# Performance work log

Hardware: AMD Instinct MI355X
Metric: run time of the kernel (lower is better)

## Reference

```python
import jax, jax.numpy as jnp
import numpy as np

N_NODES = 50000
N_EDGES = 800000
D_IN = 128
D_OUT = 128


def setup_inputs() -> dict:
    key = jax.random.key(0)
    k1, k2, k3, k4, k5 = jax.random.split(key, 5)
    gain = float(np.sqrt(2.0))  # calculate_gain('relu')
    # xavier_uniform bound: gain * sqrt(6/(fan_in+fan_out))
    bound = gain * float(np.sqrt(6.0 / (D_IN + D_OUT)))
    feat = jax.random.normal(k1, (N_NODES, D_IN), dtype=jnp.float32)
    weight = jax.random.uniform(k2, (D_IN, D_OUT), minval=-bound, maxval=bound, dtype=jnp.float32)
    loop_weight = jax.random.uniform(k3, (D_IN, D_OUT), minval=-bound, maxval=bound, dtype=jnp.float32)
    h_bias = jnp.zeros((D_OUT,), dtype=jnp.float32)
    src = jax.random.randint(k4, (N_EDGES,), 0, N_NODES, dtype=jnp.int32)
    dst = jax.random.randint(k5, (N_EDGES,), 0, N_NODES, dtype=jnp.int32)
    return {"feat": feat, "weight": weight, "h_bias": h_bias,
            "loop_weight": loop_weight, "src": src, "dst": dst}


def reference(feat, weight, h_bias, loop_weight, src, dst):
    # message: m_e = feat[src_e] @ W ; aggregate: h_v = sum_{e: dst_e=v} m_e
    # (equivalently transform-then-gather, which avoids the [E, D] matmul)
    transformed = feat @ weight                    # [N, D_out]
    msgs = transformed[src]                        # [E, D_out] gather
    h = jax.ops.segment_sum(msgs, dst, num_segments=feat.shape[0])  # [N, D_out]
    h = h + h_bias                                 # bias
    h = h + feat @ loop_weight                     # self-loop
    # activation=None, dropout=0 -> identity
    return h
```

## Files before the change

### kernel.cpp

```cpp
#include <hip/hip_runtime.h>

#define D 128
#define CAP 64

typedef __attribute__((ext_vector_type(8))) short bf16x8;
typedef __attribute__((ext_vector_type(4))) float f32x4;

__device__ inline unsigned short f2bf_rne(float x) {
    unsigned u = __float_as_uint(x);
    return (unsigned short)((u + 0x7FFFu + ((u >> 16) & 1u)) >> 16);
}

__global__ __launch_bounds__(256) void prep_kernel(
    const float* __restrict__ W, const float* __restrict__ LW,
    unsigned short* __restrict__ Bt, int* __restrict__ cursor, int N)
{
    int tid = blockIdx.x * 256 + threadIdx.x;
    if (tid < 2 * D * D) {
        int n = tid >> 7;
        int k = tid & 127;
        float v = (n < D) ? W[(size_t)k * D + n] : LW[(size_t)k * D + (n - D)];
        Bt[(size_t)n * D + k] = f2bf_rne(v);
    }
    int j = tid - 2 * D * D;
    if (j >= 0 && j < N) cursor[j] = 0;
}

__global__ __launch_bounds__(256) void mfma_transform(
    const float* __restrict__ feat, const unsigned short* __restrict__ Bt,
    const float* __restrict__ bias, unsigned short* __restrict__ T,
    float* __restrict__ out, int N)
{
    const int wave = threadIdx.x >> 6;
    const int lane = threadIdx.x & 63;
    const int row0 = blockIdx.x * 16;
    const int m    = lane & 15;
    const int kg   = lane >> 4;

    int arow_idx = row0 + m;
    if (arow_idx >= N) arow_idx = N - 1;
    const float* arow = feat + (size_t)arow_idx * D;

    bf16x8 a[4];
#pragma unroll
    for (int ks = 0; ks < 4; ++ks) {
        const float4 f0 = *(const float4*)(arow + ks * 32 + kg * 8);
        const float4 f1 = *(const float4*)(arow + ks * 32 + kg * 8 + 4);
        bf16x8 v;
        v[0] = (short)f2bf_rne(f0.x); v[1] = (short)f2bf_rne(f0.y);
        v[2] = (short)f2bf_rne(f0.z); v[3] = (short)f2bf_rne(f0.w);
        v[4] = (short)f2bf_rne(f1.x); v[5] = (short)f2bf_rne(f1.y);
        v[6] = (short)f2bf_rne(f1.z); v[7] = (short)f2bf_rne(f1.w);
        a[ks] = v;
    }

    const int colbase = wave * 64;
    f32x4 acc[4];
#pragma unroll
    for (int t = 0; t < 4; ++t) acc[t] = (f32x4){0.f, 0.f, 0.f, 0.f};

#pragma unroll
    for (int t = 0; t < 4; ++t) {
        const unsigned short* brow = Bt + (size_t)(colbase + t * 16 + m) * D;
#pragma unroll
        for (int ks = 0; ks < 4; ++ks) {
            bf16x8 b = *(const bf16x8*)(brow + ks * 32 + kg * 8);
            acc[t] = __builtin_amdgcn_mfma_f32_16x16x32_bf16(a[ks], b, acc[t], 0, 0, 0);
        }
    }

#pragma unroll
    for (int t = 0; t < 4; ++t) {
        const int col = colbase + t * 16 + m;
#pragma unroll
        for (int r = 0; r < 4; ++r) {
            const int row = row0 + kg * 4 + r;
            if (row < N) {
                const float v = acc[t][r];
                if (col < D) {
                    T[(size_t)row * D + col] = f2bf_rne(v);
                } else {
                    const int c = col - D;
                    out[(size_t)row * D + c] = v + bias[c];
                }
            }
        }
    }
}

__global__ __launch_bounds__(256) void fill_kernel(
    const int* __restrict__ src, const int* __restrict__ dst,
    int* __restrict__ cursor, unsigned short* __restrict__ ebuf, int E)
{
    int e = blockIdx.x * 256 + threadIdx.x;
    if (e >= E) return;
    const int d = dst[e];
    int pos = atomicAdd(&cursor[d], 1);
    if (pos < CAP) ebuf[(size_t)d * CAP + pos] = (unsigned short)src[e];
}

__global__ __launch_bounds__(256) void gather_kernel(
    const unsigned short* __restrict__ ebuf, const int* __restrict__ cursor,
    const unsigned short* __restrict__ T, float* __restrict__ out, int N)
{
    const int node = (blockIdx.x * 256 + threadIdx.x) >> 6;
    const int lane = threadIdx.x & 63;
    if (node >= N) return;

    int deg = cursor[node];
    if (deg > CAP) deg = CAP;

    const unsigned* region = (const unsigned*)(ebuf + (size_t)node * CAP);
    const unsigned short* Tbase = T + 2 * lane;

    float ax = 0.f, ay = 0.f;

    for (int j = 0; j < deg; j += 8) {
        unsigned w[4];
#pragma unroll
        for (int k = 0; k < 4; ++k) w[k] = region[(j >> 1) + k];

        unsigned u[8];
#pragma unroll
        for (int k = 0; k < 8; ++k) {
            const unsigned s = (k & 1) ? (w[k >> 1] >> 16) : (w[k >> 1] & 0xFFFFu);
            u[k] = *(const unsigned*)(Tbase + (size_t)s * D);
        }
#pragma unroll
        for (int k = 0; k < 8; ++k) {
            const bool live = (j + k) < deg;
            const float vx = __uint_as_float(u[k] << 16);
            const float vy = __uint_as_float(u[k] & 0xFFFF0000u);
            ax += live ? vx : 0.f;
            ay += live ? vy : 0.f;
        }
    }

    float2* o = (float2*)(out + (size_t)node * D + 2 * lane);
    float2 cur = *o;
    cur.x += ax;
    cur.y += ay;
    *o = cur;
}

extern "C" void kernel_launch(void* const* d_in, const int* in_sizes, int n_in,
                              void* d_out, int out_size, void* d_ws, size_t ws_size,
                              hipStream_t stream) {
    const float* feat = (const float*)d_in[0];
    const float* W    = (const float*)d_in[1];
    const float* bias = (const float*)d_in[2];
    const float* LW   = (const float*)d_in[3];
    const int*   src  = (const int*)d_in[4];
    const int*   dst  = (const int*)d_in[5];
    float* out = (float*)d_out;

    const int N = in_sizes[0] / D;
    const int E = in_sizes[4];

    unsigned short* T    = (unsigned short*)d_ws;
    unsigned short* Bt   = T + (size_t)N * D;
    unsigned short* ebuf = Bt + 2 * D * D;
    int* cursor = (int*)(ebuf + (size_t)N * CAP);

    {
        const int work = 2 * D * D + N;
        prep_kernel<<<dim3((work + 255) / 256), 256, 0, stream>>>(W, LW, Bt, cursor, N);
    }

    fill_kernel<<<dim3((E + 255) / 256), 256, 0, stream>>>(src, dst, cursor, ebuf, E);

    mfma_transform<<<dim3((N + 15) / 16), 256, 0, stream>>>(feat, Bt, bias, T, out, N);

    gather_kernel<<<dim3((N + 3) / 4), 256, 0, stream>>>(ebuf, cursor, T, out, N);
}
```

Measured before the change: 199.3 us.

## Merge edge fill into transform kernel and defer self-loop add to gather

The edge-bucketing fill and the MFMA transform now run as one launch: the first block range does the matmul, and the remaining blocks bucket edges. Each edge chunk is scanned by 8 blocks, and each block handles only destinations of one residue class mod 8. This spreads the cursor atomics apart, at the cost of reading dst eight times. The self-loop product is kept as bf16 next to the message transform in a 256-wide buffer, and the gather kernel adds bias and self-loop before writing out once. That removes the fp32 read-modify-write of the output but lowers the precision of the self-loop term.

```diff
diff --git a/kernel.cpp b/kernel.cpp
--- a/kernel.cpp
+++ b/kernel.cpp
@@ -2,6 +2,7 @@
 
 #define D 128
 #define CAP 64
+#define FCHUNK 2048
 
 typedef __attribute__((ext_vector_type(8))) short bf16x8;
 typedef __attribute__((ext_vector_type(4))) float f32x4;
@@ -26,82 +27,83 @@
     if (j >= 0 && j < N) cursor[j] = 0;
 }
 
-__global__ __launch_bounds__(256) void mfma_transform(
+__global__ __launch_bounds__(256) void merged_kernel(
     const float* __restrict__ feat, const unsigned short* __restrict__ Bt,
-    const float* __restrict__ bias, unsigned short* __restrict__ T,
-    float* __restrict__ out, int N)
+    unsigned short* __restrict__ T2,
+    const int* __restrict__ src, const int* __restrict__ dst,
+    int* __restrict__ cursor, unsigned short* __restrict__ ebuf,
+    int N, int E, int gb_mfma)
 {
-    const int wave = threadIdx.x >> 6;
-    const int lane = threadIdx.x & 63;
-    const int row0 = blockIdx.x * 16;
-    const int m    = lane & 15;
-    const int kg   = lane >> 4;
+    if ((int)blockIdx.x < gb_mfma) {
+        const int wave = threadIdx.x >> 6;
+        const int lane = threadIdx.x & 63;
+        const int row0 = blockIdx.x * 16;
+        const int m    = lane & 15;
+        const int kg   = lane >> 4;
 
-    int arow_idx = row0 + m;
-    if (arow_idx >= N) arow_idx = N - 1;
-    const float* arow = feat + (size_t)arow_idx * D;
+        int arow_idx = row0 + m;
+        if (arow_idx >= N) arow_idx = N - 1;
+        const float* arow = feat + (size_t)arow_idx * D;
 
-    bf16x8 a[4];
+        bf16x8 a[4];
 #pragma unroll
-    for (int ks = 0; ks < 4; ++ks) {
-        const float4 f0 = *(const float4*)(arow + ks * 32 + kg * 8);
-        const float4 f1 = *(const float4*)(arow + ks * 32 + kg * 8 + 4);
-        bf16x8 v;
-        v[0] = (short)f2bf_rne(f0.x); v[1] = (short)f2bf_rne(f0.y);
-        v[2] = (short)f2bf_rne(f0.z); v[3] = (short)f2bf_rne(f0.w);
-        v[4] = (short)f2bf_rne(f1.x); v[5] = (short)f2bf_rne(f1.y);
-        v[6] = (short)f2bf_rne(f1.z); v[7] = (short)f2bf_rne(f1.w);
-        a[ks] = v;
-    }
+        for (int ks = 0; ks < 4; ++ks) {
+            const float4 f0 = *(const float4*)(arow + ks * 32 + kg * 8);
+            const float4 f1 = *(const float4*)(arow + ks * 32 + kg * 8 + 4);
+            bf16x8 v;
+            v[0] = (short)f2bf_rne(f0.x); v[1] = (short)f2bf_rne(f0.y);
+            v[2] = (short)f2bf_rne(f0.z); v[3] = (short)f2bf_rne(f0.w);
+            v[4] = (short)f2bf_rne(f1.x); v[5] = (short)f2bf_rne(f1.y);
+            v[6] = (short)f2bf_rne(f1.z); v[7] = (short)f2bf_rne(f1.w);
+            a[ks] = v;
+        }
 
-    const int colbase = wave * 64;
-    f32x4 acc[4];
+        const int colbase = wave * 64;
+        f32x4 acc[4];
 #pragma unroll
-    for (int t = 0; t < 4; ++t) acc[t] = (f32x4){0.f, 0.f, 0.f, 0.f};
+        for (int t = 0; t < 4; ++t) acc[t] = (f32x4){0.f, 0.f, 0.f, 0.f};
 
 #pragma unroll
-    for (int t = 0; t < 4; ++t) {
-        const unsigned short* brow = Bt + (size_t)(colbase + t * 16 + m) * D;
+        for (int t = 0; t < 4; ++t) {
+            const unsigned short* brow = Bt + (size_t)(colbase + t * 16 + m) * D;
 #pragma unroll
-        for (int ks = 0; ks < 4; ++ks) {
-            bf16x8 b = *(const bf16x8*)(brow + ks * 32 + kg * 8);
-            acc[t] = __builtin_amdgcn_mfma_f32_16x16x32_bf16(a[ks], b, acc[t], 0, 0, 0);
+            for (int ks = 0; ks < 4; ++ks) {
+                bf16x8 b = *(const bf16x8*)(brow + ks * 32 + kg * 8);
+                acc[t] = __builtin_amdgcn_mfma_f32_16x16x32_bf16(a[ks], b, acc[t], 0, 0, 0);
+            }
         }
-    }
 
 #pragma unroll
-    for (int t = 0; t < 4; ++t) {
-        const int col = colbase + t * 16 + m;
+        for (int t = 0; t < 4; ++t) {
+            const int col = colbase + t * 16 + m;
 #pragma unroll
-        for (int r = 0; r < 4; ++r) {
-            const int row = row0 + kg * 4 + r;
-            if (row < N) {
-                const float v = acc[t][r];
-                if (col < D) {
-                    T[(size_t)row * D + col] = f2bf_rne(v);
-                } else {
-                    const int c = col - D;
-                    out[(size_t)row * D + c] = v + bias[c];
-                }
+            for (int r = 0; r < 4; ++r) {
+                const int row = row0 + kg * 4 + r;
+                if (row < N) T2[(size_t)row * 256 + col] = f2bf_rne(acc[t][r]);
+            }
+        }
+    } else {
+        const int fb    = (int)blockIdx.x - gb_mfma;
+        const int chunk = fb >> 3;
+        const int cls   = (int)blockIdx.x & 7;
+        const int base  = chunk * FCHUNK;
+
+        for (int i = threadIdx.x; i < FCHUNK; i += 256) {
+            const int e = base + i;
+            if (e >= E) break;
+            const int d = dst[e];
+            if ((d & 7) == cls) {
+                int pos = atomicAdd(&cursor[d], 1);
+                if (pos < CAP) ebuf[(size_t)d * CAP + pos] = (unsigned short)src[e];
             }
         }
     }
 }
 
-__global__ __launch_bounds__(256) void fill_kernel(
-    const int* __restrict__ src, const int* __restrict__ dst,
-    int* __restrict__ cursor, unsigned short* __restrict__ ebuf, int E)
-{
-    int e = blockIdx.x * 256 + threadIdx.x;
-    if (e >= E) return;
-    const int d = dst[e];
-    int pos = atomicAdd(&cursor[d], 1);
-    if (pos < CAP) ebuf[(size_t)d * CAP + pos] = (unsigned short)src[e];
-}
-
 __global__ __launch_bounds__(256) void gather_kernel(
     const unsigned short* __restrict__ ebuf, const int* __restrict__ cursor,
-    const unsigned short* __restrict__ T, float* __restrict__ out, int N)
+    const unsigned short* __restrict__ T2, const float* __restrict__ bias,
+    float* __restrict__ out, int N)
 {
     const int node = (blockIdx.x * 256 + threadIdx.x) >> 6;
     const int lane = threadIdx.x & 63;
@@ -111,7 +113,7 @@
     if (deg > CAP) deg = CAP;
 
     const unsigned* region = (const unsigned*)(ebuf + (size_t)node * CAP);
-    const unsigned short* Tbase = T + 2 * lane;
+    const unsigned short* Tbase = T2 + 2 * lane;
 
     float ax = 0.f, ay = 0.f;
 
@@ -124,23 +126,22 @@
 #pragma unroll
         for (int k = 0; k < 8; ++k) {
             const unsigned s = (k & 1) ? (w[k >> 1] >> 16) : (w[k >> 1] & 0xFFFFu);
-            u[k] = *(const unsigned*)(Tbase + (size_t)s * D);
+            u[k] = *(const unsigned*)(Tbase + (size_t)s * 256);
         }
 #pragma unroll
         for (int k = 0; k < 8; ++k) {
             const bool live = (j + k) < deg;
-            const float vx = __uint_as_float(u[k] << 16);
-            const float vy = __uint_as_float(u[k] & 0xFFFF0000u);
-            ax += live ? vx : 0.f;
-            ay += live ? vy : 0.f;
+            ax += live ? __uint_as_float(u[k] << 16) : 0.f;
+            ay += live ? __uint_as_float(u[k] & 0xFFFF0000u) : 0.f;
         }
     }
 
-    float2* o = (float2*)(out + (size_t)node * D + 2 * lane);
-    float2 cur = *o;
-    cur.x += ax;
-    cur.y += ay;
-    *o = cur;
+    const unsigned sw = *(const unsigned*)(T2 + (size_t)node * 256 + 128 + 2 * lane);
+    const float2 b = *(const float2*)(bias + 2 * lane);
+    float2 o;
+    o.x = b.x + __uint_as_float(sw << 16) + ax;
+    o.y = b.y + __uint_as_float(sw & 0xFFFF0000u) + ay;
+    *(float2*)(out + (size_t)node * D + 2 * lane) = o;
 }
 
 extern "C" void kernel_launch(void* const* d_in, const int* in_sizes, int n_in,
@@ -157,8 +158,8 @@
     const int N = in_sizes[0] / D;
     const int E = in_sizes[4];
 
-    unsigned short* T    = (unsigned short*)d_ws;
-    unsigned short* Bt   = T + (size_t)N * D;
+    unsigned short* T2   = (unsigned short*)d_ws;
+    unsigned short* Bt   = T2 + (size_t)N * 256;
     unsigned short* ebuf = Bt + 2 * D * D;
     int* cursor = (int*)(ebuf + (size_t)N * CAP);
 
@@ -167,9 +168,12 @@
         prep_kernel<<<dim3((work + 255) / 256), 256, 0, stream>>>(W, LW, Bt, cursor, N);
     }
 
-    fill_kernel<<<dim3((E + 255) / 256), 256, 0, stream>>>(src, dst, cursor, ebuf, E);
+    {
+        const int gb_mfma = (N + 15) / 16;
+        const int nchunks = (E + FCHUNK - 1) / FCHUNK;
+        merged_kernel<<<dim3(gb_mfma + nchunks * 8), 256, 0, stream>>>(
+            feat, Bt, T2, src, dst, cursor, ebuf, N, E, gb_mfma);
+    }
 
-    mfma_transform<<<dim3((N + 15) / 16), 256, 0, stream>>>(feat, Bt, bias, T, out, N);
-
-    gather_kernel<<<dim3((N + 3) / 4), 256, 0, stream>>>(ebuf, cursor, T, out, N);
+    gather_kernel<<<dim3((N + 3) / 4), 256, 0, stream>>>(ebuf, cursor, T2, bias, out, N);
 }
```

After: 189.0 us. 5.1% less time.
